# Performance work log

Hardware: AMD Instinct MI355X
Metric: run time of the kernel (lower is better)

Reference implementation:

```python
import jax, jax.numpy as jnp
import numpy as np

B, IN, H, NC = 8192, 1024, 1024, 16
CS = H // NC  # chunk_size = 64


def cumsoftmax(x):
    # cumulative softmax along last dim
    return jnp.cumsum(jax.nn.softmax(x, axis=-1), axis=-1)


def setup_inputs() -> dict:
    key = jax.random.key(0)
    ks = jax.random.split(key, 9)
    s_ih = 1.0 / np.sqrt(IN)
    s_hh = 1.0 / np.sqrt(H)
    return {
        "x": jax.random.normal(ks[0], (B, IN), jnp.float32),
        "hx": jax.random.normal(ks[1], (B, H), jnp.float32),
        "cx": jax.random.normal(ks[2], (B, NC, CS), jnp.float32),
        "input_floor": jax.random.normal(ks[3], (B, NC), jnp.float32),
        "forget_floor": jax.random.normal(ks[4], (B, NC), jnp.float32),
        "W_ih": jax.random.uniform(ks[5], (4 * H, IN), jnp.float32, -s_ih, s_ih),
        "b_ih": jax.random.uniform(ks[6], (4 * H,), jnp.float32, -s_ih, s_ih),
        "W_hh": jax.random.uniform(ks[7], (4 * H, H), jnp.float32, -s_hh, s_hh),
        "b_hh": jax.random.uniform(ks[8], (4 * H,), jnp.float32, -s_hh, s_hh),
    }


def reference(x, hx, cx, input_floor, forget_floor, W_ih, b_ih, W_hh, b_hh):
    # dual GEMM (eval path: dropconnect=0.0 -> plain linear)
    gates = x @ W_ih.T + b_ih + hx @ W_hh.T + b_hh          # [B, 4H]
    g = gates.reshape(-1, NC * 4, CS)                        # [B, 4*NC, CS]
    outgate, cell, ingate, forgetgate = jnp.split(g, 4, axis=1)  # each [B, NC, CS]

    happy_in, sad_in = jnp.split(input_floor, 2, axis=1)     # [B, NC/2] each
    happy_fg, sad_fg = jnp.split(forget_floor, 2, axis=1)

    happy_cingate = cumsoftmax(happy_in)
    happy_cforgetgate = jnp.flip(cumsoftmax(jnp.flip(happy_fg, 1)), 1)
    sad_cingate = jnp.flip(cumsoftmax(jnp.flip(sad_in, 1)), 1)
    sad_cforgetgate = cumsoftmax(sad_fg)

    cingate = jnp.concatenate([happy_cingate, sad_cingate], axis=1)[:, :, None]      # [B, NC, 1]
    cforgetgate = jnp.concatenate([happy_cforgetgate, sad_cforgetgate], axis=1)[:, :, None]

    ingate = jax.nn.sigmoid(ingate)
    forgetgate = jax.nn.sigmoid(forgetgate)
    cell = jnp.tanh(cell)
    outgate = jax.nn.sigmoid(outgate)

    overlap = cforgetgate * cingate
    forgetgate = forgetgate * overlap + (cforgetgate - overlap)
    ingate = ingate * overlap + (cingate - overlap)

    cy = forgetgate * cx + ingate * cell                     # [B, NC, CS]
    hy = outgate * jnp.tanh(cy)
    return hy.reshape(-1, H), cy
```

## Files before the change

### kernel.cpp

```cpp
#include <hip/hip_runtime.h>
#include <hip/hip_bf16.h>


#define B_ROWS 8192
#define IN_DIM 1024
#define H_DIM  1024
#define NCHUNK 16
#define K_TOT  2048

#define BM   128
#define BN   256
#define BK   64
#define NKT  (K_TOT / BK)
#define THREADS 512

#define A_PACK_BYTES ((size_t)B_ROWS * K_TOT * 2)
#define W_PACK_BYTES ((size_t)16 * 256 * K_TOT * 2)

typedef __attribute__((ext_vector_type(4))) float  f32x4;
typedef __bf16 bf16x8 __attribute__((ext_vector_type(8)));

__device__ __forceinline__ float sigmoidf_(float x) {
    return 1.0f / (1.0f + __expf(-x));
}
__device__ __forceinline__ float tanhf_(float x) {
    float e = __expf(-2.0f * fabsf(x));
    float t = (1.0f - e) / (1.0f + e);
    return copysignf(t, x);
}

__device__ __forceinline__ void gload16(const __bf16* gsrc, __bf16* lds_dst) {
    __builtin_amdgcn_global_load_lds(
        (const __attribute__((address_space(1))) unsigned int*)gsrc,
        (__attribute__((address_space(3))) unsigned int*)lds_dst, 16, 0, 0);
}

__device__ __forceinline__ bf16x8 cvt8(f32x4 v0, f32x4 v1) {
    bf16x8 o;
    o[0] = (__bf16)v0.x; o[1] = (__bf16)v0.y; o[2] = (__bf16)v0.z; o[3] = (__bf16)v0.w;
    o[4] = (__bf16)v1.x; o[5] = (__bf16)v1.y; o[6] = (__bf16)v1.z; o[7] = (__bf16)v1.w;
    return o;
}

__global__ __launch_bounds__(256)
void pack_AW(const float* __restrict__ x, const float* __restrict__ hx,
             const float* __restrict__ W_ih, const float* __restrict__ W_hh,
             __bf16* __restrict__ Abf, __bf16* __restrict__ Wp)
{
    const int bid = blockIdx.x;
    const int c8  = threadIdx.x << 3;
    if (bid < B_ROWS) {
        const float* src = (c8 < IN_DIM)
            ? (x  + (size_t)bid * IN_DIM + c8)
            : (hx + (size_t)bid * IN_DIM + (c8 - IN_DIM));
        f32x4 v0 = *reinterpret_cast<const f32x4*>(src);
        f32x4 v1 = *reinterpret_cast<const f32x4*>(src + 4);
        *reinterpret_cast<bf16x8*>(Abf + (size_t)bid * K_TOT + c8) = cvt8(v0, v1);
    } else {
        const int r  = bid - B_ROWS;
        const int bh = r >> 8;
        const int n  = r & 255;
        const int g  = (n >> 4) & 3;
        const int j  = (n >> 6) * 16 + (n & 15);
        const int wr = g * H_DIM + bh * 64 + j;
        const float* src = (c8 < IN_DIM)
            ? (W_ih + (size_t)wr * IN_DIM + c8)
            : (W_hh + (size_t)wr * IN_DIM + (c8 - IN_DIM));
        f32x4 v0 = *reinterpret_cast<const f32x4*>(src);
        f32x4 v1 = *reinterpret_cast<const f32x4*>(src + 4);
        *reinterpret_cast<bf16x8*>(Wp + (size_t)r * K_TOT + c8) = cvt8(v0, v1);
    }
}

__device__ __forceinline__ void stage_q(const __bf16* __restrict__ gbase, int kb,
                                        __bf16* lbase, int row0, int tid) {
    int e   = tid * 8;
    int row = row0 + (e >> 6);
    int kd  = e & 63;
    gload16(gbase + (size_t)row * K_TOT + kb + (kd ^ ((row & 7) << 3)), lbase + e);
}

#define SWZ(r, k) ((r) * 64 + ((k) ^ (((r) & 7) << 3)))

#define LDB(Bs) { \
    _Pragma("unroll") \
    for (int fn = 0; fn < 4; ++fn) { \
        int br = wcol + fn * 16 + lr; \
        bfr[fn][0] = *reinterpret_cast<const bf16x8*>(&(Bs)[SWZ(br, lh * 8)]); \
        bfr[fn][1] = *reinterpret_cast<const bf16x8*>(&(Bs)[SWZ(br, 32 + lh * 8)]); \
    } }

#define LDA(As, q) { \
    int ar = wrow + (q) * 16 + lr; \
    af[0] = *reinterpret_cast<const bf16x8*>(&(As)[SWZ(ar, lh * 8)]); \
    af[1] = *reinterpret_cast<const bf16x8*>(&(As)[SWZ(ar, 32 + lh * 8)]); \
    }

#define BARRIER do { \
    asm volatile("" ::: "memory"); \
    __builtin_amdgcn_s_barrier(); \
    asm volatile("" ::: "memory"); \
} while (0)

#define MF_Q(q) { \
    _Pragma("unroll") \
    for (int ks = 0; ks < 2; ++ks) { \
        _Pragma("unroll") \
        for (int fn = 0; fn < 4; ++fn) { \
            acc[q][fn] = __builtin_amdgcn_mfma_f32_16x16x32_bf16(af[ks], bfr[fn][ks], acc[q][fn], 0, 0, 0); \
        } \
    } \
}

__global__ __launch_bounds__(THREADS, 4)
void onlstm_gemm13(const __bf16* __restrict__ Abf, const __bf16* __restrict__ Wp,
                   const float* __restrict__ cx,
                   const float* __restrict__ input_floor,
                   const float* __restrict__ forget_floor,
                   const float* __restrict__ b_ih, const float* __restrict__ b_hh,
                   float* __restrict__ out)
{
    __shared__ __align__(16) __bf16 lds[24576];
    __shared__ float ci_s[BM], cf_s[BM], bias_s[BN];

    const int tid = threadIdx.x;
    const int n0  = blockIdx.x;
    const int bm  = (n0 & 7) * 8 + ((n0 >> 3) & 7);
    const int bh  = n0 >> 6;
    const int h0  = bh * 64;
    const int nc  = bh;

    if (tid < BN) {
        int g = (tid >> 4) & 3;
        int j = (tid >> 6) * 16 + (tid & 15);
        int wrr = g * H_DIM + h0 + j;
        bias_s[tid] = b_ih[wrr] + b_hh[wrr];
    }
    if (tid < BM) {
        int b = bm * BM + tid;
        const int off = (nc < 8) ? 0 : 8;
        const int ic  = (nc < 8) ? nc : (nc - 8);
        const float* pin = input_floor  + (size_t)b * NCHUNK + off;
        const float* pfg = forget_floor + (size_t)b * NCHUNK + off;
        float vi[8], vf[8];
        float mi = -1e30f, mf = -1e30f;
        #pragma unroll
        for (int t = 0; t < 8; ++t) {
            vi[t] = pin[t]; vf[t] = pfg[t];
            mi = fmaxf(mi, vi[t]); mf = fmaxf(mf, vf[t]);
        }
        float si = 0.f, sf = 0.f;
        #pragma unroll
        for (int t = 0; t < 8; ++t) {
            vi[t] = __expf(vi[t] - mi); vf[t] = __expf(vf[t] - mf);
            si += vi[t]; sf += vf[t];
        }
        float pi = 0.f, pf = 0.f;
        #pragma unroll
        for (int t = 0; t < 8; ++t) { if (t <= ic) { pi += vi[t]; pf += vf[t]; } }
        float suf_i = si - pi + vi[ic];
        float suf_f = sf - pf + vf[ic];
        float civ, cfv;
        if (nc < 8) { civ = pi / si;    cfv = suf_f / sf; }
        else        { civ = suf_i / si; cfv = pf / sf;    }
        ci_s[tid] = civ; cf_s[tid] = cfv;
    }

    const __bf16* Arow = Abf + (size_t)(bm * BM) * K_TOT;
    const __bf16* Wblk = Wp  + (size_t)bh * 256 * K_TOT;
    __bf16* const Ap = lds;
    __bf16* const Bp = lds + 8192;

    const int l    = tid & 63;
    const int wid  = tid >> 6;
    const int wrw  = wid >> 2;
    const int wc   = wid & 3;
    const int lr   = l & 15;
    const int lh   = l >> 4;
    const int wrow = wrw * 64;
    const int wcol = wc * 64;

    f32x4  acc[4][4];
    #pragma unroll
    for (int i = 0; i < 4; ++i)
        #pragma unroll
        for (int j = 0; j < 4; ++j) acc[i][j] = (f32x4){0.f, 0.f, 0.f, 0.f};
    bf16x8 af[2];
    bf16x8 bfr[4][2];

    #pragma unroll 1
    for (int t = 0; t < NKT; ++t) {
        const int kb = t * BK;
        asm volatile("s_waitcnt lgkmcnt(0)" ::: "memory");
        BARRIER;
        stage_q(Arow, kb, Ap,         0,   tid);
        stage_q(Arow, kb, Ap + 4096,  64,  tid);
        stage_q(Wblk, kb, Bp,         0,   tid);
        stage_q(Wblk, kb, Bp + 4096,  64,  tid);
        stage_q(Wblk, kb, Bp + 8192,  128, tid);
        stage_q(Wblk, kb, Bp + 12288, 192, tid);
        asm volatile("s_waitcnt vmcnt(0)" ::: "memory");
        BARRIER;
        LDB(Bp);
        LDA(Ap, 0); MF_Q(0);
        LDA(Ap, 1); MF_Q(1);
        LDA(Ap, 2); MF_Q(2);
        LDA(Ap, 3); MF_Q(3);
    }

    const size_t CY_OFF = (size_t)B_ROWS * H_DIM;
    const int hcol = h0 + wc * 16 + lr;
    #pragma unroll
    for (int m = 0; m < 4; ++m) {
        #pragma unroll
        for (int r = 0; r < 4; ++r) {
            int rt = wrow + m * 16 + lh * 4 + r;
            int b  = bm * BM + rt;
            float civ = ci_s[rt], cfv = cf_s[rt];
            float ovl = cfv * civ;
            float og = acc[m][0][r] + bias_s[wcol + lr];
            float cg = acc[m][1][r] + bias_s[wcol + 16 + lr];
            float ig = acc[m][2][r] + bias_s[wcol + 32 + lr];
            float fg = acc[m][3][r] + bias_s[wcol + 48 + lr];
            float i_s = sigmoidf_(ig);
            float f_s = sigmoidf_(fg);
            float c_t = tanhf_(cg);
            float o_s = sigmoidf_(og);
            float fq = f_s * ovl + (cfv - ovl);
            float iq = i_s * ovl + (civ - ovl);
            float cxv = cx[(size_t)b * H_DIM + hcol];
            float cyv = fq * cxv + iq * c_t;
            float hyv = o_s * tanhf_(cyv);
            out[(size_t)b * H_DIM + hcol] = hyv;
            out[CY_OFF + (size_t)b * H_DIM + hcol] = cyv;
        }
    }
}

extern "C" void kernel_launch(void* const* d_in, const int* in_sizes, int n_in,
                              void* d_out, int out_size, void* d_ws, size_t ws_size,
                              hipStream_t stream) {
    const float* x            = (const float*)d_in[0];
    const float* hx           = (const float*)d_in[1];
    const float* cx           = (const float*)d_in[2];
    const float* input_floor  = (const float*)d_in[3];
    const float* forget_floor = (const float*)d_in[4];
    const float* W_ih         = (const float*)d_in[5];
    const float* b_ih         = (const float*)d_in[6];
    const float* W_hh         = (const float*)d_in[7];
    const float* b_hh         = (const float*)d_in[8];
    float* out = (float*)d_out;

    __bf16* Abf = (__bf16*)d_ws;
    __bf16* Wp  = (__bf16*)((char*)d_ws + A_PACK_BYTES);
    pack_AW<<<B_ROWS + 16 * 256, 256, 0, stream>>>(x, hx, W_ih, W_hh, Abf, Wp);
    onlstm_gemm13<<<1024, THREADS, 0, stream>>>(
        Abf, Wp, cx, input_floor, forget_floor, b_ih, b_hh, out);
}
```

Before: 157.7 us.

## Software-pipeline GEMM K-loop with double-buffered A tiles and overlapped staging

Restructures the main K loop so global-to-LDS staging of the next tile's A (double buffered) and B (single buffer, reloaded after a barrier once its fragments are in registers) is issued while MFMAs for the current tile run. A prologue stages the first tile, and A fragments alternate between two register sets so LDS reads overlap compute. This aims to hide global load latency that the previous load-wait-compute loop exposed, at the cost of more LDS (64KB vs 48KB), which may reduce occupancy, plus more complex barrier ordering.

After: 332.1 us. 111% more time.

```diff
diff --git a/kernel.cpp b/kernel.cpp
--- a/kernel.cpp
+++ b/kernel.cpp
@@ -72,12 +72,15 @@
     }
 }
 
-__device__ __forceinline__ void stage_q(const __bf16* __restrict__ gbase, int kb,
-                                        __bf16* lbase, int row0, int tid) {
-    int e   = tid * 8;
-    int row = row0 + (e >> 6);
-    int kd  = e & 63;
-    gload16(gbase + (size_t)row * K_TOT + kb + (kd ^ ((row & 7) << 3)), lbase + e);
+__device__ __forceinline__ void stage_half(const __bf16* __restrict__ gbase, int kb,
+                                           __bf16* lbase, int row0, int tid) {
+    #pragma unroll
+    for (int i = 0; i < 2; ++i) {
+        int e   = i * 4096 + tid * 8;
+        int row = row0 + (e >> 6);
+        int kd  = e & 63;
+        gload16(gbase + (size_t)row * K_TOT + kb + (kd ^ ((row & 7) << 3)), lbase + e);
+    }
 }
 
 #define SWZ(r, k) ((r) * 64 + ((k) ^ (((r) & 7) << 3)))
@@ -90,10 +93,10 @@
         bfr[fn][1] = *reinterpret_cast<const bf16x8*>(&(Bs)[SWZ(br, 32 + lh * 8)]); \
     } }
 
-#define LDA(As, q) { \
-    int ar = wrow + (q) * 16 + lr; \
-    af[0] = *reinterpret_cast<const bf16x8*>(&(As)[SWZ(ar, lh * 8)]); \
-    af[1] = *reinterpret_cast<const bf16x8*>(&(As)[SWZ(ar, 32 + lh * 8)]); \
+#define LDA_TO(dst, As, m) { \
+    int ar = wrow + (m) * 16 + lr; \
+    dst[0] = *reinterpret_cast<const bf16x8*>(&(As)[SWZ(ar, lh * 8)]); \
+    dst[1] = *reinterpret_cast<const bf16x8*>(&(As)[SWZ(ar, 32 + lh * 8)]); \
     }
 
 #define BARRIER do { \
@@ -101,26 +104,51 @@
     __builtin_amdgcn_s_barrier(); \
     asm volatile("" ::: "memory"); \
 } while (0)
-
-#define MF_Q(q) { \
+#define LGKM0 asm volatile("s_waitcnt lgkmcnt(0)" ::: "memory")
+
+#define MF_M(m, a) { \
     _Pragma("unroll") \
     for (int ks = 0; ks < 2; ++ks) { \
         _Pragma("unroll") \
         for (int fn = 0; fn < 4; ++fn) { \
-            acc[q][fn] = __builtin_amdgcn_mfma_f32_16x16x32_bf16(af[ks], bfr[fn][ks], acc[q][fn], 0, 0, 0); \
+            acc[m][fn] = __builtin_amdgcn_mfma_f32_16x16x32_bf16(a[ks], bfr[fn][ks], acc[m][fn], 0, 0, 0); \
         } \
     } \
 }
 
+#define TILE17(T, Ac, An) { \
+    const int t_ = (T); \
+     \
+    LDB(Bp); \
+    LDA_TO(afE, Ac, 0); \
+    LDA_TO(afO, Ac, 1); \
+    stage_half(Arow, ((t_ + 1) & 31) * BK, An, 0, tid); \
+    MF_M(0, afE); \
+    BARRIER; \
+     \
+    LDA_TO(afE, Ac, 2); \
+    stage_half(Wblk, ((t_ + 1) & 31) * BK, Bp,        0,   tid); \
+    MF_M(1, afO); \
+     \
+    LDA_TO(afO, Ac, 3); \
+    stage_half(Wblk, ((t_ + 1) & 31) * BK, Bp + 8192, 128, tid); \
+    MF_M(2, afE); \
+     \
+    MF_M(3, afO); \
+    LGKM0; \
+    asm volatile("s_waitcnt vmcnt(0)" ::: "memory"); \
+    BARRIER; \
+}
+
 __global__ __launch_bounds__(THREADS, 4)
-void onlstm_gemm13(const __bf16* __restrict__ Abf, const __bf16* __restrict__ Wp,
+void onlstm_gemm17(const __bf16* __restrict__ Abf, const __bf16* __restrict__ Wp,
                    const float* __restrict__ cx,
                    const float* __restrict__ input_floor,
                    const float* __restrict__ forget_floor,
                    const float* __restrict__ b_ih, const float* __restrict__ b_hh,
                    float* __restrict__ out)
 {
-    __shared__ __align__(16) __bf16 lds[24576];
+    __shared__ __align__(16) __bf16 lds[32768];
     __shared__ float ci_s[BM], cf_s[BM], bias_s[BN];
 
     const int tid = threadIdx.x;
@@ -168,8 +196,9 @@
 
     const __bf16* Arow = Abf + (size_t)(bm * BM) * K_TOT;
     const __bf16* Wblk = Wp  + (size_t)bh * 256 * K_TOT;
-    __bf16* const Ap = lds;
-    __bf16* const Bp = lds + 8192;
+    __bf16* const A0p = lds;
+    __bf16* const A1p = lds + 8192;
+    __bf16* const Bp  = lds + 16384;
 
     const int l    = tid & 63;
     const int wid  = tid >> 6;
@@ -180,33 +209,29 @@
     const int wrow = wrw * 64;
     const int wcol = wc * 64;
 
+    stage_half(Arow, 0, A0p,        0,   tid);
+    stage_half(Wblk, 0, Bp,         0,   tid);
+    stage_half(Wblk, 0, Bp + 8192,  128, tid);
+    LGKM0;
+    asm volatile("s_waitcnt vmcnt(0)" ::: "memory");
+    __builtin_amdgcn_s_barrier();
+    asm volatile("" ::: "memory");
+
     f32x4  acc[4][4];
     #pragma unroll
     for (int i = 0; i < 4; ++i)
         #pragma unroll
         for (int j = 0; j < 4; ++j) acc[i][j] = (f32x4){0.f, 0.f, 0.f, 0.f};
-    bf16x8 af[2];
+    bf16x8 afE[2], afO[2];
     bf16x8 bfr[4][2];
 
     #pragma unroll 1
-    for (int t = 0; t < NKT; ++t) {
-        const int kb = t * BK;
-        asm volatile("s_waitcnt lgkmcnt(0)" ::: "memory");
-        BARRIER;
-        stage_q(Arow, kb, Ap,         0,   tid);
-        stage_q(Arow, kb, Ap + 4096,  64,  tid);
-        stage_q(Wblk, kb, Bp,         0,   tid);
-        stage_q(Wblk, kb, Bp + 4096,  64,  tid);
-        stage_q(Wblk, kb, Bp + 8192,  128, tid);
-        stage_q(Wblk, kb, Bp + 12288, 192, tid);
-        asm volatile("s_waitcnt vmcnt(0)" ::: "memory");
-        BARRIER;
-        LDB(Bp);
-        LDA(Ap, 0); MF_Q(0);
-        LDA(Ap, 1); MF_Q(1);
-        LDA(Ap, 2); MF_Q(2);
-        LDA(Ap, 3); MF_Q(3);
-    }
+    for (int it = 0; it < NKT / 2; ++it) {
+        const int t = 2 * it;
+        TILE17(t,     A0p, A1p);
+        TILE17(t + 1, A1p, A0p);
+    }
+    asm volatile("s_waitcnt vmcnt(0) lgkmcnt(0)" ::: "memory");
 
     const size_t CY_OFF = (size_t)B_ROWS * H_DIM;
     const int hcol = h0 + wc * 16 + lr;
@@ -254,6 +279,6 @@
     __bf16* Abf = (__bf16*)d_ws;
     __bf16* Wp  = (__bf16*)((char*)d_ws + A_PACK_BYTES);
     pack_AW<<<B_ROWS + 16 * 256, 256, 0, stream>>>(x, hx, W_ih, W_hh, Abf, Wp);
-    onlstm_gemm13<<<1024, THREADS, 0, stream>>>(
+    onlstm_gemm17<<<1024, THREADS, 0, stream>>>(
         Abf, Wp, cx, input_floor, forget_floor, b_ih, b_hh, out);
 }
```
